# Optimization experiments

Measured on AMD Instinct MI355X. Metric: run time of the kernel, lower is better.

The kernel has to match this reference:

```python
import jax, jax.numpy as jnp
import numpy as np

ACTIVE_VOCAB = 8192  # current_size == init_vocab (eval mode, no growth)
EPS = 1e-12


def _l2_normalize(v, axis=-1):
    n = jnp.sqrt(jnp.sum(v * v, axis=axis, keepdims=True))
    return v / jnp.maximum(n, EPS)


def setup_inputs() -> dict:
    key = jax.random.key(0)
    k1, k2 = jax.random.split(key)
    B, T, D, V = 8, 2048, 512, 16384
    x = jax.random.normal(k1, (B, T, D), dtype=jnp.float32)
    codebook = jax.random.normal(k2, (V, D), dtype=jnp.float32) * (D ** -0.5)
    return {"x": x, "codebook": codebook}


def reference(x, codebook):
    B, T, D = x.shape
    x_flat = x.reshape(-1, D)                      # (N, D), N = B*T
    x_norm = _l2_normalize(x_flat)
    cb_active = codebook[:ACTIVE_VOCAB]            # (V, D)
    cb_norm = _l2_normalize(cb_active)
    # cosine similarities, compute-heavy GEMM (N x D x V)
    sims = jnp.einsum("nd,vd->nv", x_norm, cb_norm)
    indices = jnp.argmax(sims, axis=-1)            # (N,)
    max_sims = jnp.max(sims, axis=-1)              # (N,)
    # codebook gather (embedding lookup)
    z_q_flat = cb_active[indices]                  # (N, D)
    z_q = z_q_flat.reshape(B, T, D)
    # straight-through estimator
    z_q_ste = x + jax.lax.stop_gradient(z_q - x)
    # usage entropy over active codes
    N = B * T
    counts = jnp.zeros(ACTIVE_VOCAB, jnp.float32).at[indices].add(1.0)
    probs = counts / (N + 1e-9)
    usage_entropy = -jnp.sum(jnp.where(probs > 0, probs * jnp.log(jnp.maximum(probs, EPS)), 0.0))
    mean_sim = jnp.mean(max_sims)
    return z_q_ste, indices.reshape(B, T), usage_entropy, mean_sim
```

## Files before the change

kernel.cpp:

```cpp
#include <hip/hip_runtime.h>

typedef short bf16x8 __attribute__((ext_vector_type(8)));
typedef float f32x4  __attribute__((ext_vector_type(4)));

#define NROW  16384
#define DD    512
#define VOCAB 8192
#define VS    4
#define VCH   2048
#define BM    256
#define BN    256
#define BK    64
#define NCHUNK 8
#define NKT    8
#define NTILE  64

#define CBBF_W   4194304
#define CANDV_W  6291456
#define CANDI_W  6815744
#define OUT_IDX  ((size_t)NROW * DD)
#define OUT_ENT  (OUT_IDX + NROW)
#define OUT_MEAN (OUT_ENT + 1)

#define WS_CBNORM 0
#define WS_MAXSIM 16384
#define WS_COUNTS 32768
#define WS_CANDV  49152
#define WS_CANDI  311296
#define WS_NEED_BYTES ((size_t)(311296 + 262144) * 4)

#define GLD_LDS(g, l) \
    __builtin_amdgcn_global_load_lds((const __attribute__((address_space(1))) void*)(g), \
                                     (__attribute__((address_space(3))) void*)(l), 16, 0, 0)

#define BAR()   __builtin_amdgcn_s_barrier()
#define LGKM0() asm volatile("s_waitcnt lgkmcnt(0)" ::: "memory")
#define VM10()  asm volatile("s_waitcnt vmcnt(10)" ::: "memory")
#define VM6()   asm volatile("s_waitcnt vmcnt(6)" ::: "memory")
#define VM0()   asm volatile("s_waitcnt vmcnt(0)" ::: "memory")

__device__ __forceinline__ ushort f2bf(float f) {
    unsigned u = __float_as_uint(f);
    return (ushort)((u + 0x7fffu + ((u >> 16) & 1u)) >> 16);
}

__global__ void eq_prep(const float* __restrict__ x, const float* __restrict__ cb,
                        ushort* __restrict__ xbf, ushort* __restrict__ cbbf,
                        float* __restrict__ nrm, int* __restrict__ counts) {
    const int b = blockIdx.x;
    const int tid = threadIdx.x;
    if (b < 4096) {
        size_t i = ((size_t)b * 256 + tid) * 8;
        float4 v0 = *(const float4*)(x + i);
        float4 v1 = *(const float4*)(x + i + 4);
        ushort r[8] = {f2bf(v0.x), f2bf(v0.y), f2bf(v0.z), f2bf(v0.w),
                       f2bf(v1.x), f2bf(v1.y), f2bf(v1.z), f2bf(v1.w)};
        *(uint4*)(xbf + i) = *(const uint4*)r;
        return;
    }
    const int bb = b - 4096;
    if (bb < 32) counts[bb * 256 + tid] = 0;
    const int row = bb * 4 + (tid >> 6);
    const int l = tid & 63;
    const float* p = cb + (size_t)row * DD;
    float4 a = *(const float4*)(p + l * 4);
    float4 bq = *(const float4*)(p + 256 + l * 4);
    float s = a.x * a.x + a.y * a.y + a.z * a.z + a.w * a.w
            + bq.x * bq.x + bq.y * bq.y + bq.z * bq.z + bq.w * bq.w;
#pragma unroll
    for (int off = 32; off > 0; off >>= 1) s += __shfl_xor(s, off, 64);
    float n = fmaxf(sqrtf(s), 1e-12f);
    float rn = 1.0f / n;
    ushort r0[4] = {f2bf(a.x * rn), f2bf(a.y * rn), f2bf(a.z * rn), f2bf(a.w * rn)};
    ushort r1[4] = {f2bf(bq.x * rn), f2bf(bq.y * rn), f2bf(bq.z * rn), f2bf(bq.w * rn)};
    *(uint2*)(cbbf + (size_t)row * DD + l * 4)       = *(const uint2*)r0;
    *(uint2*)(cbbf + (size_t)row * DD + 256 + l * 4) = *(const uint2*)r1;
    if (l == 0) nrm[row] = n;
}

__global__ __launch_bounds__(512, 2) void eq_gemm_topk(
    const ushort* __restrict__ xbf, const ushort* __restrict__ cbbf,
    float* __restrict__ candval, int* __restrict__ candidx) {
    __shared__ __align__(16) char LDS[131072];
    const int tid = threadIdx.x;
    const int lane = tid & 63;
    const int w = tid >> 6;
    const int wm = w >> 2;
    const int wn = w & 3;
    const int c = lane & 15, q = lane >> 4;

    const int bid = blockIdx.x;
    const int vsplit = (bid & 7) >> 1;
    const int xtile  = ((bid >> 3) << 1) | (bid & 1);
    const int xbase  = xtile * BN;
    const int vsbase = vsplit * VCH;

    const char* gA = (const char*)cbbf + (size_t)vsbase * 1024;
    const char* gB = (const char*)xbf  + (size_t)xbase  * 1024;
    const int thrOff = (w * 32 + (lane >> 2)) * 1024
                     + ((((lane & 3) ^ ((lane >> 3) & 3))) << 4);
    const int wp0 = w * 2048;
    const int rdsw = (q ^ ((c >> 1) & 3)) << 4;
    const int aoff = (wm * 128 + c) * 64 + rdsw;
    const int boff = 65536 + (wn * 64 + c) * 64 + rdsw;

#define STAGE_A(lin2, h) do { int _l = (lin2); if (_l < NTILE) { \
        const char* _s = gA + ((_l >> 3) * 262144 + (_l & 7) * 128 + (h) * 64) + thrOff; \
        char* _d = (char*)LDS + ((_l & 1) * 32768 + (h) * 16384 + wp0); \
        GLD_LDS(_s, _d); GLD_LDS(_s + 16384, _d + 1024); } } while (0)
#define STAGE_B(lin2, h) do { int _l = (lin2); if (_l < NTILE) { \
        const char* _s = gB + ((_l & 7) * 128 + (h) * 64) + thrOff; \
        char* _d = (char*)LDS + (65536 + (_l & 1) * 32768 + (h) * 16384 + wp0); \
        GLD_LDS(_s, _d); GLD_LDS(_s + 16384, _d + 1024); } } while (0)

    int t1k[4], t2k[4];
#pragma unroll
    for (int nj = 0; nj < 4; ++nj) { t1k[nj] = 0x80000000; t2k[nj] = 0x80000000; }

    f32x4 acc[8][4];

    STAGE_A(0, 0); STAGE_B(0, 0); STAGE_A(0, 1); STAGE_B(0, 1);
    STAGE_A(1, 0); STAGE_B(1, 0); STAGE_A(1, 1);
    VM6(); BAR();

    for (int lin = 0; lin < NTILE; ++lin) {
        const int set = (lin & 1) * 32768;
        if ((lin & 7) == 0) {
#pragma unroll
            for (int mi = 0; mi < 8; ++mi)
#pragma unroll
                for (int nj = 0; nj < 4; ++nj) acc[mi][nj] = (f32x4){0.f, 0.f, 0.f, 0.f};
        }
        bf16x8 af[8], bf0, bf1;
#pragma unroll
        for (int mi = 0; mi < 8; ++mi)
            af[mi] = *(const bf16x8*)(LDS + set + aoff + mi * 1024);
        bf0 = *(const bf16x8*)(LDS + set + boff);
        bf1 = *(const bf16x8*)(LDS + set + boff + 1024);
        STAGE_B(lin + 1, 1);
        BAR(); LGKM0();
        __builtin_amdgcn_s_setprio(1);
#pragma unroll
        for (int mi = 0; mi < 8; ++mi) {
            acc[mi][0] = __builtin_amdgcn_mfma_f32_16x16x32_bf16(af[mi], bf0, acc[mi][0], 0, 0, 0);
            acc[mi][1] = __builtin_amdgcn_mfma_f32_16x16x32_bf16(af[mi], bf1, acc[mi][1], 0, 0, 0);
        }
        __builtin_amdgcn_s_setprio(0);
        BAR();
        bf0 = *(const bf16x8*)(LDS + set + boff + 2048);
        bf1 = *(const bf16x8*)(LDS + set + boff + 3072);
        STAGE_A(lin + 2, 0);
        if (lin < 62) { VM10(); } else { VM0(); }
        BAR(); LGKM0();
        __builtin_amdgcn_s_setprio(1);
#pragma unroll
        for (int mi = 0; mi < 8; ++mi) {
            acc[mi][2] = __builtin_amdgcn_mfma_f32_16x16x32_bf16(af[mi], bf0, acc[mi][2], 0, 0, 0);
            acc[mi][3] = __builtin_amdgcn_mfma_f32_16x16x32_bf16(af[mi], bf1, acc[mi][3], 0, 0, 0);
        }
        __builtin_amdgcn_s_setprio(0);
        BAR();
#pragma unroll
        for (int mi = 0; mi < 8; ++mi)
            af[mi] = *(const bf16x8*)(LDS + set + 16384 + aoff + mi * 1024);
        bf0 = *(const bf16x8*)(LDS + set + 16384 + boff);
        bf1 = *(const bf16x8*)(LDS + set + 16384 + boff + 1024);
        STAGE_B(lin + 2, 0);
        BAR(); LGKM0();
        __builtin_amdgcn_s_setprio(1);
#pragma unroll
        for (int mi = 0; mi < 8; ++mi) {
            acc[mi][0] = __builtin_amdgcn_mfma_f32_16x16x32_bf16(af[mi], bf0, acc[mi][0], 0, 0, 0);
            acc[mi][1] = __builtin_amdgcn_mfma_f32_16x16x32_bf16(af[mi], bf1, acc[mi][1], 0, 0, 0);
        }
        __builtin_amdgcn_s_setprio(0);
        BAR();
        bf0 = *(const bf16x8*)(LDS + set + 16384 + boff + 2048);
        bf1 = *(const bf16x8*)(LDS + set + 16384 + boff + 3072);
        STAGE_A(lin + 2, 1);
        if (lin < 62) { VM10(); } else { VM0(); }
        BAR(); LGKM0();
        __builtin_amdgcn_s_setprio(1);
#pragma unroll
        for (int mi = 0; mi < 8; ++mi) {
            acc[mi][2] = __builtin_amdgcn_mfma_f32_16x16x32_bf16(af[mi], bf0, acc[mi][2], 0, 0, 0);
            acc[mi][3] = __builtin_amdgcn_mfma_f32_16x16x32_bf16(af[mi], bf1, acc[mi][3], 0, 0, 0);
        }
        __builtin_amdgcn_s_setprio(0);
        BAR();
        if ((lin & 7) == 7) {
            const int chb = (lin >> 3) << 5;
#pragma unroll
            for (int nj = 0; nj < 4; ++nj)
#pragma unroll
                for (int mi = 0; mi < 8; ++mi)
#pragma unroll
                    for (int r = 0; r < 4; ++r) {
                        int key = (__float_as_int(acc[mi][nj][r]) & (int)0xFFFFFF00)
                                | (chb + mi * 4 + r);
                        int mn = t1k[nj] < key ? t1k[nj] : key;
                        t1k[nj] = t1k[nj] < key ? key : t1k[nj];
                        t2k[nj] = t2k[nj] < mn ? mn : t2k[nj];
                    }
        }
    }
#pragma unroll
    for (int nj = 0; nj < 4; ++nj) {
        int k1 = t1k[nj], k2 = t2k[nj];
        float t1v = __int_as_float(k1 & (int)0xFFFFFF00);
        float t2v = __int_as_float(k2 & (int)0xFFFFFF00);
        int l1 = k1 & 255, l2 = k2 & 255;
        int t1i = vsbase + ((l1 >> 5) << 8) + (wm << 7) + (((l1 >> 2) & 7) << 4) + (q << 2) + (l1 & 3);
        int t2i = vsbase + ((l2 >> 5) << 8) + (wm << 7) + (((l2 >> 2) & 7) << 4) + (q << 2) + (l2 & 3);
#pragma unroll
        for (int off = 16; off <= 32; off <<= 1) {
            float o1v = __shfl_xor(t1v, off, 64); int o1i = __shfl_xor(t1i, off, 64);
            float o2v = __shfl_xor(t2v, off, 64); int o2i = __shfl_xor(t2i, off, 64);
            bool wbest = (t1v > o1v) || (t1v == o1v && t1i < o1i);
            float m1 = wbest ? t1v : o1v;  int m1i = wbest ? t1i : o1i;
            float ca = wbest ? o1v : t1v;  int cai = wbest ? o1i : t1i;
            float cw = wbest ? t2v : o2v;  int cwi = wbest ? t2i : o2i;
            bool s2 = (ca > cw) || (ca == cw && cai < cwi);
            t1v = m1;           t1i = m1i;
            t2v = s2 ? ca : cw; t2i = s2 ? cai : cwi;
        }
        if (q == 0) {
            int list = vsplit * 2 + wm;
            int row = xbase + wn * 64 + nj * 16 + c;
            size_t base = ((size_t)list * NROW + row) * 2;
            candval[base] = t1v; candval[base + 1] = t2v;
            candidx[base] = t1i; candidx[base + 1] = t2i;
        }
    }
#undef STAGE_A
#undef STAGE_B
}

template <bool FUSE_ZQ>
__device__ __forceinline__ void rescore_body(
    const float* __restrict__ x, const float* __restrict__ cb,
    const float* __restrict__ cbnorm,
    const float* __restrict__ candval, const int* __restrict__ candidx,
    float* __restrict__ out, float* __restrict__ maxsim, int* __restrict__ counts) {
    int w = threadIdx.x >> 6, l = threadIdx.x & 63;
    int row = blockIdx.x * 4 + w;

    const float4* X4 = (const float4*)(x + (size_t)row * DD);
    float4 xa = X4[l], xb = X4[l + 64];
    float s2 = xa.x * xa.x + xa.y * xa.y + xa.z * xa.z + xa.w * xa.w
             + xb.x * xb.x + xb.y * xb.y + xb.z * xb.z + xb.w * xb.w;
#pragma unroll
    for (int off = 32; off > 0; off >>= 1) s2 += __shfl_xor(s2, off, 64);
    float xn = fmaxf(sqrtf(s2), 1e-12f);
    double xd[8] = {(double)(xa.x / xn), (double)(xa.y / xn), (double)(xa.z / xn),
                    (double)(xa.w / xn), (double)(xb.x / xn), (double)(xb.y / xn),
                    (double)(xb.z / xn), (double)(xb.w / xn)};

    float cv[16]; int ci[16];
#pragma unroll
    for (int t = 0; t < 16; ++t) {
        size_t b = ((size_t)(t >> 1) * NROW + row) * 2 + (t & 1);
        cv[t] = candval[b]; ci[t] = candidx[b];
    }
    float bv1 = cv[0];
#pragma unroll
    for (int t = 1; t < 16; ++t) bv1 = fmaxf(bv1, cv[t]);
    float margin = 2e-3f * xn;

    double best = -1e300; int bi = 1 << 30;
    for (int t = 0; t < 16; ++t) {
        if (cv[t] >= bv1 - margin) {
            float n = cbnorm[ci[t]];
            const float4* C4 = (const float4*)(cb + (size_t)ci[t] * DD);
            float4 ca = C4[l], cb4 = C4[l + 64];
            double a = xd[0] * (double)(ca.x / n) + xd[1] * (double)(ca.y / n)
                     + xd[2] * (double)(ca.z / n) + xd[3] * (double)(ca.w / n)
                     + xd[4] * (double)(cb4.x / n) + xd[5] * (double)(cb4.y / n)
                     + xd[6] * (double)(cb4.z / n) + xd[7] * (double)(cb4.w / n);
#pragma unroll
            for (int off = 32; off > 0; off >>= 1) a += __shfl_xor(a, off, 64);
            bool better = (a > best) || (a == best && ci[t] < bi);
            best = better ? a : best;
            bi = better ? ci[t] : bi;
        }
    }
    if (l == 0) {
        out[OUT_IDX + row] = (float)bi;
        maxsim[row] = (float)best;
        atomicAdd(counts + bi, 1);
    }
    if (FUSE_ZQ) {
        const float4* src = (const float4*)(cb + (size_t)bi * DD);
        float4* dst = (float4*)(out + (size_t)row * DD);
        dst[l] = src[l];
        dst[l + 64] = src[l + 64];
    }
}

__global__ void eq_rescore(const float* __restrict__ x, const float* __restrict__ cb,
                           const float* __restrict__ cbnorm,
                           const float* __restrict__ candval, const int* __restrict__ candidx,
                           float* __restrict__ out, float* __restrict__ maxsim,
                           int* __restrict__ counts) {
    rescore_body<false>(x, cb, cbnorm, candval, candidx, out, maxsim, counts);
}

__global__ void eq_rescore_fused(const float* __restrict__ x, const float* __restrict__ cb,
                                 const float* __restrict__ cbnorm,
                                 const float* __restrict__ candval, const int* __restrict__ candidx,
                                 float* __restrict__ out, float* __restrict__ maxsim,
                                 int* __restrict__ counts) {
    rescore_body<true>(x, cb, cbnorm, candval, candidx, out, maxsim, counts);
}

__global__ void eq_gather(const float* __restrict__ cb, float* __restrict__ out) {
    int w = threadIdx.x >> 6, l = threadIdx.x & 63;
    int row = blockIdx.x * 4 + w;
    int bi = (int)out[OUT_IDX + row];
    const float4* src = (const float4*)(cb + (size_t)bi * DD);
    float4* dst = (float4*)(out + (size_t)row * DD);
    dst[l] = src[l];
    dst[l + 64] = src[l + 64];
}

__global__ void eq_entropy_mean(const int* __restrict__ counts,
                                const float* __restrict__ maxsim,
                                float* __restrict__ out) {
    __shared__ float red[16];
    int tid = threadIdx.x;
    float s = 0.f;
    for (int b = tid; b < VOCAB; b += 1024) {
        int c = counts[b];
        if (c > 0) {
            float p = (float)c * (1.0f / 16384.0f);
            s += p * logf(p);
        }
    }
#pragma unroll
    for (int off = 32; off > 0; off >>= 1) s += __shfl_down(s, off, 64);
    if ((tid & 63) == 0) red[tid >> 6] = s;
    __syncthreads();
    if (tid == 0) {
        float t = 0.f;
#pragma unroll
        for (int i = 0; i < 16; ++i) t += red[i];
        out[OUT_ENT] = -t;
    }
    __syncthreads();
    float m = 0.f;
    for (int i = tid; i < NROW; i += 1024) m += maxsim[i];
#pragma unroll
    for (int off = 32; off > 0; off >>= 1) m += __shfl_down(m, off, 64);
    if ((tid & 63) == 0) red[tid >> 6] = m;
    __syncthreads();
    if (tid == 0) {
        float t = 0.f;
#pragma unroll
        for (int i = 0; i < 16; ++i) t += red[i];
        out[OUT_MEAN] = t * (1.0f / 16384.0f);
    }
}

extern "C" void kernel_launch(void* const* d_in, const int* in_sizes, int n_in,
                              void* d_out, int out_size, void* d_ws, size_t ws_size,
                              hipStream_t stream) {
    const float* x  = (const float*)d_in[0];
    const float* cb = (const float*)d_in[1];
    float* out = (float*)d_out;
    float* wsf = (float*)d_ws;
    int*   wsi = (int*)d_ws;

    float* cbnorm = wsf + WS_CBNORM;
    float* maxsim = wsf + WS_MAXSIM;
    int*   counts = wsi + WS_COUNTS;

    ushort* xbf   = (ushort*)out;
    ushort* cbbf  = (ushort*)(out + CBBF_W);

    const bool fused = ws_size >= WS_NEED_BYTES;
    float* candv = fused ? (wsf + WS_CANDV) : (out + CANDV_W);
    int*   candi = fused ? (wsi + WS_CANDI) : (int*)(out + CANDI_W);

    eq_prep<<<6144, 256, 0, stream>>>(x, cb, xbf, cbbf, cbnorm, counts);

    eq_gemm_topk<<<256, 512, 0, stream>>>(xbf, cbbf, candv, candi);

    if (fused) {
        eq_rescore_fused<<<NROW / 4, 256, 0, stream>>>(x, cb, cbnorm, candv, candi,
                                                       out, maxsim, counts);
    } else {
        eq_rescore<<<NROW / 4, 256, 0, stream>>>(x, cb, cbnorm, candv, candi,
                                                 out, maxsim, counts);
        eq_gather<<<NROW / 4, 256, 0, stream>>>(cb, out);
    }
    eq_entropy_mean<<<1, 1024, 0, stream>>>(counts, maxsim, out);
}
```

Measured before the change: 262.0 us.

## Switch LDS tile layout to 128-byte rows with 8-way XOR swizzle and regroup staging

Changes the LDS layout of the A and B tiles from 64-byte half-K rows to full 128-byte K rows with an 8-way XOR swizzle. Fragment reads use new offsets, and the global-to-LDS loads now cover row halves rather than K halves. The prefetch schedule is reordered: both B halves are staged in the first two phases, both A halves together in the last phase, with a single vmcnt(4) wait per tile. The aim is fewer LDS bank conflicts and a simpler pipeline. The risk is less even load issue across the phases, and correctness depends on the new index arithmetic.

Measured after the change: 255.3 us. 1.03x faster.

```diff
diff --git a/kernel.cpp b/kernel.cpp
--- a/kernel.cpp
+++ b/kernel.cpp
@@ -35,8 +35,7 @@
 
 #define BAR()   __builtin_amdgcn_s_barrier()
 #define LGKM0() asm volatile("s_waitcnt lgkmcnt(0)" ::: "memory")
-#define VM10()  asm volatile("s_waitcnt vmcnt(10)" ::: "memory")
-#define VM6()   asm volatile("s_waitcnt vmcnt(6)" ::: "memory")
+#define VM4()   asm volatile("s_waitcnt vmcnt(4)" ::: "memory")
 #define VM0()   asm volatile("s_waitcnt vmcnt(0)" ::: "memory")
 
 __device__ __forceinline__ ushort f2bf(float f) {
@@ -97,21 +96,25 @@
 
     const char* gA = (const char*)cbbf + (size_t)vsbase * 1024;
     const char* gB = (const char*)xbf  + (size_t)xbase  * 1024;
-    const int thrOff = (w * 32 + (lane >> 2)) * 1024
-                     + ((((lane & 3) ^ ((lane >> 3) & 3))) << 4);
-    const int wp0 = w * 2048;
-    const int rdsw = (q ^ ((c >> 1) & 3)) << 4;
-    const int aoff = (wm * 128 + c) * 64 + rdsw;
-    const int boff = 65536 + (wn * 64 + c) * 64 + rdsw;
+    const int thrOff = (w * 8 + (lane >> 3)) * 1024
+                     + (((lane & 7) ^ ((lane >> 3) & 7)) << 4);
+    const int wbase = w * 1024;
+    const int sw0 = (q ^ (c & 7)) << 4;
+    const int sw1 = ((4 + q) ^ (c & 7)) << 4;
+    const int aoff0 = wm * 16384 + c * 128 + sw0;
+    const int aoff1 = wm * 16384 + c * 128 + sw1;
+    const int bbase = 65536 + (wn >> 1) * 16384 + ((wn & 1) * 64 + c) * 128;
+    const int boff0 = bbase + sw0;
+    const int boff1 = bbase + sw1;
 
 #define STAGE_A(lin2, h) do { int _l = (lin2); if (_l < NTILE) { \
-        const char* _s = gA + ((_l >> 3) * 262144 + (_l & 7) * 128 + (h) * 64) + thrOff; \
-        char* _d = (char*)LDS + ((_l & 1) * 32768 + (h) * 16384 + wp0); \
-        GLD_LDS(_s, _d); GLD_LDS(_s + 16384, _d + 1024); } } while (0)
+        const char* _s = gA + ((_l >> 3) * 262144 + (h) * 131072 + (_l & 7) * 128) + thrOff; \
+        char* _d = (char*)LDS + ((_l & 1) * 32768 + (h) * 16384 + wbase); \
+        GLD_LDS(_s, _d); GLD_LDS(_s + 65536, _d + 8192); } } while (0)
 #define STAGE_B(lin2, h) do { int _l = (lin2); if (_l < NTILE) { \
-        const char* _s = gB + ((_l & 7) * 128 + (h) * 64) + thrOff; \
-        char* _d = (char*)LDS + (65536 + (_l & 1) * 32768 + (h) * 16384 + wp0); \
-        GLD_LDS(_s, _d); GLD_LDS(_s + 16384, _d + 1024); } } while (0)
+        const char* _s = gB + ((h) * 131072 + (_l & 7) * 128) + thrOff; \
+        char* _d = (char*)LDS + (65536 + (_l & 1) * 32768 + (h) * 16384 + wbase); \
+        GLD_LDS(_s, _d); GLD_LDS(_s + 65536, _d + 8192); } } while (0)
 
     int t1k[4], t2k[4];
 #pragma unroll
@@ -119,9 +122,10 @@
 
     f32x4 acc[8][4];
 
-    STAGE_A(0, 0); STAGE_B(0, 0); STAGE_A(0, 1); STAGE_B(0, 1);
-    STAGE_A(1, 0); STAGE_B(1, 0); STAGE_A(1, 1);
-    VM6(); BAR();
+    STAGE_A(0, 0); STAGE_A(0, 1);
+    STAGE_B(0, 0); STAGE_B(0, 1);
+    STAGE_A(1, 0); STAGE_A(1, 1);
+    VM4(); BAR();
 
     for (int lin = 0; lin < NTILE; ++lin) {
         const int set = (lin & 1) * 32768;
@@ -134,38 +138,36 @@
         bf16x8 af[8], bf0, bf1;
 #pragma unroll
         for (int mi = 0; mi < 8; ++mi)
-            af[mi] = *(const bf16x8*)(LDS + set + aoff + mi * 1024);
-        bf0 = *(const bf16x8*)(LDS + set + boff);
-        bf1 = *(const bf16x8*)(LDS + set + boff + 1024);
+            af[mi] = *(const bf16x8*)(LDS + set + aoff0 + mi * 2048);
+        bf0 = *(const bf16x8*)(LDS + set + boff0);
+        bf1 = *(const bf16x8*)(LDS + set + boff0 + 2048);
+        STAGE_B(lin + 1, 0);
+        BAR(); LGKM0();
+        __builtin_amdgcn_s_setprio(1);
+#pragma unroll
+        for (int mi = 0; mi < 8; ++mi) {
+            acc[mi][0] = __builtin_amdgcn_mfma_f32_16x16x32_bf16(af[mi], bf0, acc[mi][0], 0, 0, 0);
+            acc[mi][1] = __builtin_amdgcn_mfma_f32_16x16x32_bf16(af[mi], bf1, acc[mi][1], 0, 0, 0);
+        }
+        __builtin_amdgcn_s_setprio(0);
+        BAR();
+        bf0 = *(const bf16x8*)(LDS + set + boff0 + 4096);
+        bf1 = *(const bf16x8*)(LDS + set + boff0 + 6144);
         STAGE_B(lin + 1, 1);
         BAR(); LGKM0();
         __builtin_amdgcn_s_setprio(1);
 #pragma unroll
         for (int mi = 0; mi < 8; ++mi) {
-            acc[mi][0] = __builtin_amdgcn_mfma_f32_16x16x32_bf16(af[mi], bf0, acc[mi][0], 0, 0, 0);
-            acc[mi][1] = __builtin_amdgcn_mfma_f32_16x16x32_bf16(af[mi], bf1, acc[mi][1], 0, 0, 0);
+            acc[mi][2] = __builtin_amdgcn_mfma_f32_16x16x32_bf16(af[mi], bf0, acc[mi][2], 0, 0, 0);
+            acc[mi][3] = __builtin_amdgcn_mfma_f32_16x16x32_bf16(af[mi], bf1, acc[mi][3], 0, 0, 0);
         }
         __builtin_amdgcn_s_setprio(0);
         BAR();
-        bf0 = *(const bf16x8*)(LDS + set + boff + 2048);
-        bf1 = *(const bf16x8*)(LDS + set + boff + 3072);
-        STAGE_A(lin + 2, 0);
-        if (lin < 62) { VM10(); } else { VM0(); }
-        BAR(); LGKM0();
-        __builtin_amdgcn_s_setprio(1);
-#pragma unroll
-        for (int mi = 0; mi < 8; ++mi) {
-            acc[mi][2] = __builtin_amdgcn_mfma_f32_16x16x32_bf16(af[mi], bf0, acc[mi][2], 0, 0, 0);
-            acc[mi][3] = __builtin_amdgcn_mfma_f32_16x16x32_bf16(af[mi], bf1, acc[mi][3], 0, 0, 0);
-        }
-        __builtin_amdgcn_s_setprio(0);
-        BAR();
 #pragma unroll
         for (int mi = 0; mi < 8; ++mi)
-            af[mi] = *(const bf16x8*)(LDS + set + 16384 + aoff + mi * 1024);
-        bf0 = *(const bf16x8*)(LDS + set + 16384 + boff);
-        bf1 = *(const bf16x8*)(LDS + set + 16384 + boff + 1024);
-        STAGE_B(lin + 2, 0);
+            af[mi] = *(const bf16x8*)(LDS + set + aoff1 + mi * 2048);
+        bf0 = *(const bf16x8*)(LDS + set + boff1);
+        bf1 = *(const bf16x8*)(LDS + set + boff1 + 2048);
         BAR(); LGKM0();
         __builtin_amdgcn_s_setprio(1);
 #pragma unroll
@@ -175,10 +177,11 @@
         }
         __builtin_amdgcn_s_setprio(0);
         BAR();
-        bf0 = *(const bf16x8*)(LDS + set + 16384 + boff + 2048);
-        bf1 = *(const bf16x8*)(LDS + set + 16384 + boff + 3072);
+        bf0 = *(const bf16x8*)(LDS + set + boff1 + 4096);
+        bf1 = *(const bf16x8*)(LDS + set + boff1 + 6144);
+        STAGE_A(lin + 2, 0);
         STAGE_A(lin + 2, 1);
-        if (lin < 62) { VM10(); } else { VM0(); }
+        if (lin < 62) { VM4(); } else { VM0(); }
         BAR(); LGKM0();
         __builtin_amdgcn_s_setprio(1);
 #pragma unroll
```
